# Performance work log

Measured on AMD Instinct MI355X. Metric: run time of the kernel, lower is better.

The kernel has to match this reference:

```python
import jax, jax.numpy as jnp
import numpy as np
import math

B, T, C, H, LC, DFF = 2, 1024, 1024, 16, 256, 4096
EPS = 1e-6


def _ln(x):
    # LayerNorm without affine (elementwise_affine=False under AdaLN), eps=1e-6
    m = jnp.mean(x, -1, keepdims=True)
    v = jnp.mean((x - m) ** 2, -1, keepdims=True)
    return (x - m) * jax.lax.rsqrt(v + EPS)


def _heads(t):
    b, l, c = t.shape
    return t.reshape(b, l, H, c // H).transpose(0, 2, 1, 3)  # (b,H,l,dh)


def _unheads(t):
    b, h, l, d = t.shape
    return t.transpose(0, 2, 1, 3).reshape(b, l, h * d)


def setup_inputs():
    key = jax.random.key(0)
    ks = jax.random.split(key, 16)
    s = 0.02
    p = lambda k, sh: jax.random.normal(k, sh, jnp.float32) * s
    x_star = jax.random.normal(ks[0], (B, T, C), jnp.float32)
    x_hat = jax.random.normal(ks[1], (B, T, C), jnp.float32)
    c = jax.random.normal(ks[2], (B, LC, C), jnp.float32)
    chunk = jnp.sort(jax.random.randint(ks[3], (B, T), 0, 32), axis=1)
    m_star = chunk[:, :, None] > chunk[:, None, :]   # attend to strictly earlier chunks
    m_hat = chunk[:, :, None] == chunk[:, None, :]   # attend within same chunk
    dep_mask = jax.random.bernoulli(ks[4], 0.98, (B, T, T)) | jnp.eye(T, dtype=bool)[None]
    return dict(
        x_star=x_star, x_hat=x_hat, c=c,
        m_star=m_star, m_hat=m_hat, dep_mask=dep_mask,
        ncond_g=jnp.ones((C,), jnp.float32), ncond_b=jnp.zeros((C,), jnp.float32),
        Wq=p(ks[5], (C, C)), bq=jnp.zeros((C,), jnp.float32),
        Wkv=p(ks[6], (C, 2 * C)), bkv=jnp.zeros((2 * C,), jnp.float32),
        Wco=p(ks[7], (C, C)), bco=jnp.zeros((C,), jnp.float32),
        Wada=p(ks[8], (C, 6 * C)), bada=jnp.zeros((6 * C,), jnp.float32),
        Wqkv=p(ks[9], (C, 3 * C)), bqkv=jnp.zeros((3 * C,), jnp.float32),
        Wo=p(ks[10], (C, C)), bo=jnp.zeros((C,), jnp.float32),
        W1=p(ks[11], (C, DFF)), b1=jnp.zeros((DFF,), jnp.float32),
        W2=p(ks[12], (DFF, C)), b2=jnp.zeros((C,), jnp.float32),
    )


def _cross_attn(x, c, Wq, bq, Wkv, bkv, Wco, bco):
    q = _heads(x @ Wq + bq)
    k, v = jnp.split(c @ Wkv + bkv, 2, -1)
    k, v = _heads(k), _heads(v)
    att = jnp.einsum('bhtd,bhsd->bhts', q, k) / math.sqrt(C // H)
    y = jnp.einsum('bhts,bhsd->bhtd', jax.nn.softmax(att, -1), v)
    return _unheads(y) @ Wco + bco


def _interleave(xs, xh, m_star, m_hat, dep, Wqkv, bqkv, Wo, bo):
    # Attention.forward_interleave (eval: dropout identity)
    NEG = -jnp.inf
    sc = 1.0 / math.sqrt(C // H)
    qkv = lambda x: [_heads(t) for t in jnp.split(x @ Wqkv + bqkv, 3, -1)]
    qs, ks, vs = qkv(xs)
    qh, kh, vh = qkv(xh)
    blk_star = (~m_star)[:, None]     # True -> block
    blk_hat = (~m_hat)[:, None]
    blk_dep = (~dep)[:, None]
    causal = jnp.triu(jnp.ones((T, T), bool), 1)[None, None]
    # star stream: causal + dependency mask
    att_star = jnp.einsum('bhtd,bhsd->bhts', qs, ks) * sc
    att_star = jnp.where(blk_dep, NEG, att_star)
    p_star = jax.nn.softmax(jnp.where(causal, NEG, att_star), -1)
    y_star = _unheads(jnp.einsum('bhts,bhsd->bhtd', p_star, vs)) @ Wo + bo
    # hat stream: merge logits (q_hat vs k_star on earlier chunks, q_hat vs k_hat within chunk)
    a1 = jnp.where(blk_star, NEG, jnp.einsum('bhtd,bhsd->bhts', qh, ks) * sc)
    a2 = jnp.where(blk_hat, NEG, jnp.einsum('bhtd,bhsd->bhts', qh, kh) * sc)
    merged = jnp.where(jnp.isinf(a2), a1, a2)
    merged = jnp.where(blk_dep, NEG, merged)
    p_hat = jax.nn.softmax(merged, -1)
    y_hat = jnp.einsum('bhts,bhsd->bhtd', jnp.where(blk_star, 0.0, p_hat), vs) \
          + jnp.einsum('bhts,bhsd->bhtd', jnp.where(blk_hat, 0.0, p_hat), vh)
    y_hat = _unheads(y_hat) @ Wo + bo
    return y_star, y_hat


def reference(x_star, x_hat, c, m_star, m_hat, dep_mask,
              ncond_g, ncond_b, Wq, bq, Wkv, bkv, Wco, bco, Wada, bada,
              Wqkv, bqkv, Wo, bo, W1, b1, W2, b2):
    mod = lambda x, sh, scale: x * (1 + scale) + sh
    mlp = lambda x: jax.nn.gelu(x @ W1 + b1, approximate=True) @ W2 + b2
    ca = lambda x: _cross_attn(_ln(x) * ncond_g + ncond_b, c, Wq, bq, Wkv, bkv, Wco, bco)
    ada = lambda t: jnp.split(jax.nn.silu(t) @ Wada + bada, 6, -1)
    gs = ada(ca(x_star))
    gh = ada(ca(x_hat))
    ms = mod(_ln(x_star), gs[0], gs[1])
    mh = mod(_ln(x_hat), gh[0], gh[1])
    ys, yh = _interleave(ms, mh, m_star, m_hat, dep_mask, Wqkv, bqkv, Wo, bo)
    x_star = x_star + gs[2] * ys
    x_hat = x_hat + gh[2] * yh
    x_star = x_star + gs[5] * mlp(mod(_ln(x_star), gs[3], gs[4]))
    x_hat = x_hat + gh[5] * mlp(mod(_ln(x_hat), gh[3], gh[4]))
    return x_star, x_hat
```

## Files before the change

### kernel.cpp

```cpp
#include <hip/hip_runtime.h>
#include <hip/hip_bf16.h>
#include <stdint.h>

#define DEVI __device__ __forceinline__

typedef __bf16 bf16x8 __attribute__((ext_vector_type(8)));
typedef float f32x4 __attribute__((ext_vector_type(4)));
typedef unsigned short us;
typedef unsigned long long ull;

DEVI float b2f(us u) { union { unsigned int i; float f; } v; v.i = ((unsigned int)u) << 16; return v.f; }
DEVI us f2b(float f) {
  union { unsigned int i; float f; } v; v.f = f;
  unsigned int r = (v.i + 0x7fffu + ((v.i >> 16) & 1u)) >> 16;
  return (us)r;
}

#define NEGINF (-__builtin_inff())

DEVI void gl2lds16(const us* g, us* l) {
  __builtin_amdgcn_global_load_lds(
      (const __attribute__((address_space(1))) unsigned int*)g,
      (__attribute__((address_space(3))) unsigned int*)l, 16, 0, 0);
}

__global__ __launch_bounds__(256) void detect_flags(
    const unsigned int* __restrict__ xw, const unsigned int* __restrict__ mw,
    int* __restrict__ flags) {
  const int t = threadIdx.x;
  int cnt = 0, big = 0;
  for (int i = t; i < 4096; i += 256) {
    unsigned int w = xw[i];
    us lo = (us)(w & 0xffffu);
    float a = fabsf(b2f(lo));
    cnt += ((lo == 0) || (a >= 1e-8f && a <= 256.f)) ? 1 : 0;
    big |= (mw[i] > 1u) ? 1 : 0;
  }
  for (int o = 32; o; o >>= 1) { cnt += __shfl_down(cnt, o); big |= __shfl_down(big, o); }
  __shared__ int sc[4], sb[4];
  if ((t & 63) == 0) { sc[t >> 6] = cnt; sb[t >> 6] = big; }
  __syncthreads();
  if (t == 0) {
    flags[0] = (sc[0] + sc[1] + sc[2] + sc[3] < 2048) ? 1 : 0;
    flags[1] = (sb[0] | sb[1] | sb[2] | sb[3]);
  }
}

__global__ __launch_bounds__(256) void cvt_bf16(
    const void* __restrict__ src, us* __restrict__ dst, int n,
    const int* __restrict__ flags) {
  const int f32mode = flags[0];
  int idx = (blockIdx.x * 256 + threadIdx.x) * 4;
  if (idx >= n) return;
  if (f32mode) {
    const float* s = (const float*)src;
    float4 v = *(const float4*)(s + idx);
    dst[idx] = f2b(v.x); dst[idx + 1] = f2b(v.y);
    dst[idx + 2] = f2b(v.z); dst[idx + 3] = f2b(v.w);
  } else {
    *(uint2*)(dst + idx) = *(const uint2*)((const us*)src + idx);
  }
}

struct P10 { const void* p[10]; };
__global__ __launch_bounds__(256) void cvt_small(P10 ps, us* __restrict__ dst,
                                                 const int* __restrict__ flags) {
  const int offs[11] = {0, 1024, 2048, 3072, 5120, 6144, 12288, 15360, 16384, 20480, 21504};
  int idx = blockIdx.x * 256 + threadIdx.x;
  if (idx >= 21504) return;
  int seg = 0;
#pragma unroll
  for (int i = 1; i < 10; ++i) seg += (idx >= offs[i]) ? 1 : 0;
  int local = idx - offs[seg];
  float v = flags[0] ? ((const float*)ps.p[seg])[local]
                     : b2f(((const us*)ps.p[seg])[local]);
  dst[idx] = f2b(v);
}

__global__ __launch_bounds__(256) void transpose_cvt64(
    const void* __restrict__ W, us* __restrict__ WT, int K, int N,
    const int* __restrict__ flags) {
  __shared__ __attribute__((aligned(16))) us tile[64 * 72];
  const int f32m = flags[0];
  const int k0 = blockIdx.x * 64, n0 = blockIdx.y * 64;
  const int t = threadIdx.x;
  const int row = t >> 2, colb = (t & 3) * 16;
  const int sw = ((row >> 4) & 3) << 4;
  us tmp[16];
  if (f32m) {
    const float* src = (const float*)W + (size_t)(k0 + row) * N + n0 + colb;
#pragma unroll
    for (int i = 0; i < 16; i += 4) {
      float4 v = *(const float4*)(src + i);
      tmp[i] = f2b(v.x); tmp[i + 1] = f2b(v.y); tmp[i + 2] = f2b(v.z); tmp[i + 3] = f2b(v.w);
    }
  } else {
    const us* src = (const us*)W + (size_t)(k0 + row) * N + n0 + colb;
    *(uint4*)tmp = *(const uint4*)src;
    *(uint4*)(tmp + 8) = *(const uint4*)(src + 8);
  }
  *(uint4*)&tile[row * 72 + (colb ^ sw)] = *(uint4*)tmp;
  *(uint4*)&tile[row * 72 + (colb ^ sw) + 8] = *(uint4*)(tmp + 8);
  __syncthreads();
  const int orow = t >> 2, ocolb = (t & 3) * 16;
  const int pc = (orow & 15) | ((orow & 48) ^ (ocolb & 48));
  us out[16];
#pragma unroll
  for (int i = 0; i < 16; ++i) out[i] = tile[(ocolb + i) * 72 + pc];
  us* dst = WT + (size_t)(n0 + orow) * K + k0 + ocolb;
  *(uint4*)dst = *(uint4*)out;
  *(uint4*)(dst + 8) = *(uint4*)(out + 8);
}

struct P3 { const void* p[3]; };
__global__ __launch_bounds__(256) void pack_mask3(P3 ms, ull* __restrict__ bits,
                                                  const int* __restrict__ flags) {
  const int bytemode = flags[1];
  const void* m = ms.p[blockIdx.y];
  ull* out = bits + (size_t)blockIdx.y * 32768;
  int wv = blockIdx.x * 4 + (threadIdx.x >> 6);
  int lane = threadIdx.x & 63;
  for (int w = 0; w < 16; ++w) {
    int v;
    if (bytemode) v = ((const unsigned char*)m)[(size_t)wv * 1024 + w * 64 + lane];
    else          v = ((const int*)m)[(size_t)wv * 1024 + w * 64 + lane];
    ull b = __ballot(v != 0);
    if (lane == 0) out[(size_t)wv * 16 + w] = b;
  }
}

__global__ __launch_bounds__(256) void hat_blockflags(
    const ull* __restrict__ starb, const ull* __restrict__ hatb, int* __restrict__ bf) {
  const int bt = blockIdx.x;
  const int b = bt >> 4, tt = bt & 15;
  const int t = threadIdx.x, wv = t >> 6, lane = t & 63;
  const int t0 = tt * 64;
  for (int k = 0; k < 4; ++k) {
    int ck = wv * 4 + k;
    ull sw = starb[(size_t)(b * 1024 + t0 + lane) * 16 + ck];
    ull hw = hatb[(size_t)(b * 1024 + t0 + lane) * 16 + ck];
    int f = (__ballot(sw != 0ull) ? 1 : 0) | (__ballot(hw != 0ull) ? 2 : 0);
    if (lane == 0) bf[bt * 16 + ck] = f;
  }
}

__global__ __launch_bounds__(256) void vtrans(
    const us* __restrict__ src, us* __restrict__ dst,
    int T, int stride, int colBase, int rowOff) {
  __shared__ __attribute__((aligned(16))) us tile[64][65];
  const int bh = blockIdx.y, b = bh >> 4, h = bh & 15;
  const int t0 = blockIdx.x * 64;
  const int t = threadIdx.x;
#pragma unroll
  for (int it = 0; it < 2; ++it) {
    int idx = it * 256 + t; int r = idx >> 3, c8 = (idx & 7) * 8;
    uint4 d4 = *(const uint4*)(src + (size_t)(rowOff + b * T + t0 + r) * stride + colBase + h * 64 + c8);
    const us* e = (const us*)&d4;
#pragma unroll
    for (int i = 0; i < 8; ++i) tile[r][c8 + i] = e[i];
  }
  __syncthreads();
#pragma unroll
  for (int it = 0; it < 2; ++it) {
    int idx = it * 256 + t; int d = idx >> 3, c8 = (idx & 7) * 8;
    us tmp[8];
#pragma unroll
    for (int i = 0; i < 8; ++i) tmp[i] = tile[c8 + i][d];
    *(uint4*)(dst + ((size_t)(bh * 64 + d)) * T + t0 + c8) = *(const uint4*)tmp;
  }
}

__global__ __launch_bounds__(256) void ln_affine(
    const void* __restrict__ xs, const void* __restrict__ xh,
    const us* __restrict__ gw, const us* __restrict__ bw,
    us* __restrict__ lnx, us* __restrict__ xn, const int* __restrict__ flags) {
  const int f32m = flags[0];
  const int row = blockIdx.x;
  const void* xp = (row < 2048) ? xs : xh;
  const size_t base = (size_t)(row & 2047) * 1024;
  const int t = threadIdx.x;
  float v[4]; float s = 0.f, ss = 0.f;
#pragma unroll
  for (int i = 0; i < 4; ++i) {
    size_t idx = base + i * 256 + t;
    float x = f32m ? ((const float*)xp)[idx] : b2f(((const us*)xp)[idx]);
    v[i] = x; s += x; ss += x * x;
  }
  for (int o = 32; o; o >>= 1) { s += __shfl_down(s, o); ss += __shfl_down(ss, o); }
  __shared__ float red[2][4];
  const int wv = t >> 6, lane = t & 63;
  if (lane == 0) { red[0][wv] = s; red[1][wv] = ss; }
  __syncthreads();
  s = red[0][0] + red[0][1] + red[0][2] + red[0][3];
  ss = red[1][0] + red[1][1] + red[1][2] + red[1][3];
  const float mean = s * (1.f / 1024.f);
  const float var = fmaxf(ss * (1.f / 1024.f) - mean * mean, 0.f);
  const float rstd = rsqrtf(var + 1e-6f);
  const size_t ro = (size_t)row * 1024;
#pragma unroll
  for (int i = 0; i < 4; ++i) {
    int c = i * 256 + t;
    float n = (v[i] - mean) * rstd;
    lnx[ro + c] = f2b(n);
    xn[ro + c] = f2b(n * b2f(gw[c]) + b2f(bw[c]));
  }
}

__global__ __launch_bounds__(256) void mod_ms(
    const us* __restrict__ lnx, const us* __restrict__ gada, us* __restrict__ ms) {
  const size_t idx = ((size_t)blockIdx.x * 256 + threadIdx.x) * 4;
  const int row = (int)(idx >> 10), c = (int)(idx & 1023);
  const size_t gb = (size_t)row * 6144;
#pragma unroll
  for (int i = 0; i < 4; ++i) {
    float sh = b2f(gada[gb + c + i]);
    float sc = b2f(gada[gb + 1024 + c + i]);
    ms[idx + i] = f2b(b2f(lnx[idx + i]) * (1.f + sc) + sh);
  }
}

__global__ __launch_bounds__(256) void ln_mod(
    const float* __restrict__ x1, const us* __restrict__ gada, us* __restrict__ m2) {
  const int row = blockIdx.x;
  const float* xp = x1 + (size_t)row * 1024;
  const int t = threadIdx.x;
  float v[4]; float s = 0.f, ss = 0.f;
#pragma unroll
  for (int i = 0; i < 4; ++i) { float x = xp[i * 256 + t]; v[i] = x; s += x; ss += x * x; }
  for (int o = 32; o; o >>= 1) { s += __shfl_down(s, o); ss += __shfl_down(ss, o); }
  __shared__ float red[2][4];
  const int wv = t >> 6, lane = t & 63;
  if (lane == 0) { red[0][wv] = s; red[1][wv] = ss; }
  __syncthreads();
  s = red[0][0] + red[0][1] + red[0][2] + red[0][3];
  ss = red[1][0] + red[1][1] + red[1][2] + red[1][3];
  const float mean = s * (1.f / 1024.f);
  const float var = fmaxf(ss * (1.f / 1024.f) - mean * mean, 0.f);
  const float rstd = rsqrtf(var + 1e-6f);
  const size_t gb = (size_t)row * 6144;
#pragma unroll
  for (int i = 0; i < 4; ++i) {
    int c = i * 256 + t;
    float n = (v[i] - mean) * rstd;
    float sh = b2f(gada[gb + 3072 + c]);
    float sc = b2f(gada[gb + 4096 + c]);
    m2[(size_t)row * 1024 + c] = f2b(n * (1.f + sc) + sh);
  }
}

enum { EPI_BF16 = 0, EPI_SILU, EPI_GELU, EPI_GATE_XRES, EPI_GATE_OUT };

template <int EPI>
DEVI void gemm_epi(float v, int gmr, int gn, int N, void* out,
                   const us* gate, const void* res0, const void* res1,
                   const int* oflags) {
  const size_t oi = (size_t)gmr * N + gn;
  if constexpr (EPI == EPI_BF16) {
    ((us*)out)[oi] = f2b(v);
  } else if constexpr (EPI == EPI_SILU) {
    ((us*)out)[oi] = f2b(v / (1.f + __expf(-v)));
  } else if constexpr (EPI == EPI_GELU) {
    float u = 0.7978845608028654f * (v + 0.044715f * v * v * v);
    float th = 1.f - 2.f / (__expf(2.f * u) + 1.f);
    ((us*)out)[oi] = f2b(0.5f * v * (1.f + th));
  } else if constexpr (EPI == EPI_GATE_XRES) {
    float g = b2f(gate[(size_t)gmr * 6144 + gn]);
    const void* xr = (gmr < 2048) ? res0 : res1;
    size_t xi = (size_t)(gmr & 2047) * 1024 + gn;
    float x = oflags[0] ? ((const float*)xr)[xi] : b2f(((const us*)xr)[xi]);
    ((float*)out)[oi] = x + g * v;
  } else {
    float g = b2f(gate[(size_t)gmr * 6144 + gn]);
    float x = ((const float*)res0)[oi];
    float r2 = x + g * v;
    if (oflags[0]) ((float*)out)[oi] = r2;
    else ((us*)out)[oi] = f2b(r2);
  }
}

template <int EPI>
__global__ __launch_bounds__(256) void gemm_bt(
    const us* __restrict__ A, const us* __restrict__ BT,
    const us* __restrict__ bias, void* __restrict__ out,
    int M, int N, int K,
    const us* __restrict__ gate,
    const void* __restrict__ res0, const void* __restrict__ res1,
    const int* __restrict__ oflags) {
  __shared__ __attribute__((aligned(16))) us As[2][128 * 32];
  __shared__ __attribute__((aligned(16))) us Bs[2][128 * 32];
  const int m0 = blockIdx.x * 128, n0 = blockIdx.y * 128;
  const int t = threadIdx.x;
  const int wave = t >> 6, lane = t & 63;
  const int wm = (wave >> 1) * 64, wn = (wave & 1) * 64;
  const int l16 = lane & 15, quad = lane >> 4;
  f32x4 acc[4][4] = {};

  const int lr = lane >> 2, lc = (lane & 3) * 8;
  const us* gA = A + (size_t)(m0 + wave * 32 + lr) * K + lc;
  const us* gB = BT + (size_t)(n0 + wave * 32 + lr) * K + lc;
  const int wo = wave * 1024;

#define STAGE_BT(buf, k)                                    \
  { us* pA = &As[buf][wo]; us* pB = &Bs[buf][wo];           \
    gl2lds16(gA + (k), pA);                                 \
    gl2lds16(gA + (size_t)16 * K + (k), pA + 512);          \
    gl2lds16(gB + (k), pB);                                 \
    gl2lds16(gB + (size_t)16 * K + (k), pB + 512); }

  STAGE_BT(0, 0);
  STAGE_BT(1, 32);
  const int NK = K >> 5;
  int cur = 0;
  for (int i = 0; i < NK - 1; ++i) {
    asm volatile("s_waitcnt vmcnt(4)\n\ts_barrier" ::: "memory");
    bf16x8 af[4], bfv[4];
#pragma unroll
    for (int x = 0; x < 4; ++x) af[x] = *(const bf16x8*)(const void*)&As[cur][(wm + x * 16 + l16) * 32 + quad * 8];
#pragma unroll
    for (int j = 0; j < 4; ++j) bfv[j] = *(const bf16x8*)(const void*)&Bs[cur][(wn + j * 16 + l16) * 32 + quad * 8];
    asm volatile("s_waitcnt lgkmcnt(0)\n\ts_barrier" ::: "memory");
    if (i + 2 < NK) STAGE_BT(cur, (i + 2) * 32);
#pragma unroll
    for (int x = 0; x < 4; ++x)
#pragma unroll
      for (int j = 0; j < 4; ++j)
        acc[x][j] = __builtin_amdgcn_mfma_f32_16x16x32_bf16(af[x], bfv[j], acc[x][j], 0, 0, 0);
    cur ^= 1;
  }
  asm volatile("s_waitcnt vmcnt(0)\n\ts_barrier" ::: "memory");
  {
    bf16x8 af[4], bfv[4];
#pragma unroll
    for (int x = 0; x < 4; ++x) af[x] = *(const bf16x8*)(const void*)&As[cur][(wm + x * 16 + l16) * 32 + quad * 8];
#pragma unroll
    for (int j = 0; j < 4; ++j) bfv[j] = *(const bf16x8*)(const void*)&Bs[cur][(wn + j * 16 + l16) * 32 + quad * 8];
#pragma unroll
    for (int x = 0; x < 4; ++x)
#pragma unroll
      for (int j = 0; j < 4; ++j)
        acc[x][j] = __builtin_amdgcn_mfma_f32_16x16x32_bf16(af[x], bfv[j], acc[x][j], 0, 0, 0);
  }
#undef STAGE_BT

#pragma unroll
  for (int i = 0; i < 4; ++i) {
    const int gm = m0 + wm + i * 16 + quad * 4;
#pragma unroll
    for (int j = 0; j < 4; ++j) {
      const int gn = n0 + wn + j * 16 + l16;
      const float bv = b2f(bias[gn]);
#pragma unroll
      for (int r = 0; r < 4; ++r)
        gemm_epi<EPI>(acc[i][j][r] + bv, gm + r, gn, N, out, gate, res0, res1, oflags);
    }
  }
}

template <int EPI>
__global__ __launch_bounds__(256) void gemm_bt64(
    const us* __restrict__ A, const us* __restrict__ BT,
    const us* __restrict__ bias, void* __restrict__ out,
    int M, int N, int K,
    const us* __restrict__ gate,
    const void* __restrict__ res0, const void* __restrict__ res1,
    const int* __restrict__ oflags) {
  __shared__ __attribute__((aligned(16))) us As[2][128 * 32];
  __shared__ __attribute__((aligned(16))) us Bs[2][64 * 32];
  const int m0 = blockIdx.x * 128, n0 = blockIdx.y * 64;
  const int t = threadIdx.x;
  const int wave = t >> 6, lane = t & 63;
  const int wm = (wave >> 1) * 64, wn = (wave & 1) * 32;
  const int l16 = lane & 15, quad = lane >> 4;
  f32x4 acc[4][2] = {};

  const int lr = lane >> 2, lc = (lane & 3) * 8;
  const us* gA = A + (size_t)(m0 + wave * 32 + lr) * K + lc;
  const us* gB = BT + (size_t)(n0 + wave * 16 + lr) * K + lc;
  const int woA = wave * 1024, woB = wave * 512;

#define STAGE_BT64(buf, k)                                  \
  { us* pA = &As[buf][woA];                                 \
    gl2lds16(gA + (k), pA);                                 \
    gl2lds16(gA + (size_t)16 * K + (k), pA + 512);          \
    gl2lds16(gB + (k), &Bs[buf][woB]); }

  STAGE_BT64(0, 0);
  STAGE_BT64(1, 32);
  const int NK = K >> 5;
  int cur = 0;
  for (int i = 0; i < NK - 1; ++i) {
    asm volatile("s_waitcnt vmcnt(3)\n\ts_barrier" ::: "memory");
    bf16x8 af[4], bfv[2];
#pragma unroll
    for (int x = 0; x < 4; ++x) af[x] = *(const bf16x8*)(const void*)&As[cur][(wm + x * 16 + l16) * 32 + quad * 8];
#pragma unroll
    for (int j = 0; j < 2; ++j) bfv[j] = *(const bf16x8*)(const void*)&Bs[cur][(wn + j * 16 + l16) * 32 + quad * 8];
    asm volatile("s_waitcnt lgkmcnt(0)\n\ts_barrier" ::: "memory");
    if (i + 2 < NK) STAGE_BT64(cur, (i + 2) * 32);
#pragma unroll
    for (int x = 0; x < 4; ++x)
#pragma unroll
      for (int j = 0; j < 2; ++j)
        acc[x][j] = __builtin_amdgcn_mfma_f32_16x16x32_bf16(af[x], bfv[j], acc[x][j], 0, 0, 0);
    cur ^= 1;
  }
  asm volatile("s_waitcnt vmcnt(0)\n\ts_barrier" ::: "memory");
  {
    bf16x8 af[4], bfv[2];
#pragma unroll
    for (int x = 0; x < 4; ++x) af[x] = *(const bf16x8*)(const void*)&As[cur][(wm + x * 16 + l16) * 32 + quad * 8];
#pragma unroll
    for (int j = 0; j < 2; ++j) bfv[j] = *(const bf16x8*)(const void*)&Bs[cur][(wn + j * 16 + l16) * 32 + quad * 8];
#pragma unroll
    for (int x = 0; x < 4; ++x)
#pragma unroll
      for (int j = 0; j < 2; ++j)
        acc[x][j] = __builtin_amdgcn_mfma_f32_16x16x32_bf16(af[x], bfv[j], acc[x][j], 0, 0, 0);
  }
#undef STAGE_BT64

#pragma unroll
  for (int i = 0; i < 4; ++i) {
    const int gm = m0 + wm + i * 16 + quad * 4;
#pragma unroll
    for (int j = 0; j < 2; ++j) {
      const int gn = n0 + wn + j * 16 + l16;
      const float bv = b2f(bias[gn]);
#pragma unroll
      for (int r = 0; r < 4; ++r)
        gemm_epi<EPI>(acc[i][j][r] + bv, gm + r, gn, N, out, gate, res0, res1, oflags);
    }
  }
}

struct AttnState { float m[4], l[4]; f32x4 o[4]; };

DEVI void st_init(AttnState& s) {
#pragma unroll
  for (int r = 0; r < 4; ++r) { s.m[r] = NEGINF; s.l[r] = 0.f; s.o[r] = f32x4{}; }
}

DEVI void stage64(us* __restrict__ dst, const us* __restrict__ src,
                  int strideUs, int t) {
#pragma unroll
  for (int it = 0; it < 2; ++it) {
    const int id = it * 256 + t;
    const int row = id >> 3, c8 = (id & 7) * 8;
    *(uint4*)&dst[row * 72 + c8] = *(const uint4*)(src + (size_t)row * strideUs + c8);
  }
}

template <bool MASKED>
DEVI void attn_round(const us* __restrict__ Kb, const us* __restrict__ Vb,
                     us* __restrict__ Pb, const ull* mrow,
                     bf16x8 aq0, bf16x8 aq1, AttnState& st,
                     int wv, int l16, int quad) {
  f32x4 s[4];
  __builtin_amdgcn_s_setprio(1);
#pragma unroll
  for (int j = 0; j < 4; ++j) {
    const int row = j * 16 + l16;
    bf16x8 bk0 = *(const bf16x8*)(const void*)&Kb[row * 72 + quad * 8];
    bf16x8 bk1 = *(const bf16x8*)(const void*)&Kb[row * 72 + 32 + quad * 8];
    f32x4 z = {};
    z = __builtin_amdgcn_mfma_f32_16x16x32_bf16(aq0, bk0, z, 0, 0, 0);
    z = __builtin_amdgcn_mfma_f32_16x16x32_bf16(aq1, bk1, z, 0, 0, 0);
    s[j] = z;
  }
  __builtin_amdgcn_s_setprio(0);
  const float CE = 0.18033688011112042f;
#pragma unroll
  for (int r = 0; r < 4; ++r) {
    float mx = fmaxf(fmaxf(s[0][r], s[1][r]), fmaxf(s[2][r], s[3][r]));
#pragma unroll
    for (int o2 = 8; o2; o2 >>= 1) mx = fmaxf(mx, __shfl_xor(mx, o2));
    const float mn = fmaxf(st.m[r], mx);
    const float alpha = exp2f((st.m[r] - mn) * CE);
    const float mnC = mn * CE;
    float rs = 0.f;
#pragma unroll
    for (int j = 0; j < 4; ++j) {
      float p = exp2f(__builtin_fmaf(s[j][r], CE, -mnC));
      if constexpr (MASKED) p = ((mrow[r] >> (j * 16 + l16)) & 1ull) ? p : 0.f;
      rs += p;
      ((__bf16*)Pb)[(wv * 16 + quad * 4 + r) * 72 + j * 16 + l16] = (__bf16)p;
    }
#pragma unroll
    for (int o2 = 8; o2; o2 >>= 1) rs += __shfl_xor(rs, o2);
    st.m[r] = mn;
    st.l[r] = st.l[r] * alpha + rs;
#pragma unroll
    for (int jd = 0; jd < 4; ++jd) st.o[jd][r] *= alpha;
  }
  bf16x8 ap0 = *(const bf16x8*)(const void*)&Pb[(wv * 16 + l16) * 72 + quad * 8];
  bf16x8 ap1 = *(const bf16x8*)(const void*)&Pb[(wv * 16 + l16) * 72 + 32 + quad * 8];
  __builtin_amdgcn_s_setprio(1);
#pragma unroll
  for (int jd = 0; jd < 4; ++jd) {
    bf16x8 v0 = *(const bf16x8*)(const void*)&Vb[(jd * 16 + l16) * 72 + quad * 8];
    bf16x8 v1 = *(const bf16x8*)(const void*)&Vb[(jd * 16 + l16) * 72 + 32 + quad * 8];
    st.o[jd] = __builtin_amdgcn_mfma_f32_16x16x32_bf16(ap0, v0, st.o[jd], 0, 0, 0);
    st.o[jd] = __builtin_amdgcn_mfma_f32_16x16x32_bf16(ap1, v1, st.o[jd], 0, 0, 0);
  }
  __builtin_amdgcn_s_setprio(0);
}

DEVI void attn_write(us* __restrict__ y, const AttnState& st, int rowAbs,
                     int h, int l16, int quad) {
#pragma unroll
  for (int r = 0; r < 4; ++r) {
    const float inv = (st.l[r] > 0.f) ? 1.f / st.l[r] : 0.f;
#pragma unroll
    for (int jd = 0; jd < 4; ++jd)
      y[(size_t)(rowAbs + quad * 4 + r) * 1024 + h * 64 + jd * 16 + l16] =
          f2b(st.o[jd][r] * inv);
  }
}

__global__ __launch_bounds__(256) void cross_attn_mfma(
    const us* __restrict__ q, const us* __restrict__ kv,
    const us* __restrict__ vT, us* __restrict__ y) {
  __shared__ __attribute__((aligned(16))) us Kb[64 * 72];
  __shared__ __attribute__((aligned(16))) us Vb[64 * 72];
  __shared__ __attribute__((aligned(16))) us Pb[64 * 72];
  const int bid = blockIdx.x;
  const int xcd = bid & 7, tmp = bid >> 3;
  const int tt = tmp & 15, gq = tmp >> 4;
  const int g = gq * 8 + xcd;
  const int strm = g >> 5, b = (g >> 4) & 1, h = g & 15;
  const int t = threadIdx.x, wv = t >> 6, lane = t & 63;
  const int l16 = lane & 15, quad = lane >> 4;
  const int rowbase = strm * 2048 + b * 1024 + tt * 64 + wv * 16;
  const us* qp = q + (size_t)(rowbase + l16) * 1024 + h * 64 + quad * 8;
  bf16x8 aq0 = *(const bf16x8*)(qp);
  bf16x8 aq1 = *(const bf16x8*)(qp + 32);
  const us* kb = kv + (size_t)b * (256 * 2048) + h * 64;
  const us* vb = vT + (size_t)(b * 16 + h) * (64 * 256);
  AttnState st; st_init(st);
  for (int rnd = 0; rnd < 4; ++rnd) {
    const int s0 = rnd * 64;
    __syncthreads();
    stage64(Kb, kb + (size_t)s0 * 2048, 2048, t);
    stage64(Vb, vb + s0, 256, t);
    __syncthreads();
    attn_round<false>(Kb, Vb, Pb, nullptr, aq0, aq1, st, wv, l16, quad);
  }
  attn_write(y, st, rowbase, h, l16, quad);
}

DEVI void star_body(us* Kb, us* Vb, us* Pb, const us* qkv, const us* vT,
                    const ull* depb, us* y, int b, int h, int tt, int t) {
  const int wv = t >> 6, lane = t & 63;
  const int l16 = lane & 15, quad = lane >> 4;
  const int t0 = tt * 64;
  const int rowbase = b * 1024 + t0 + wv * 16;
  const us* qp = qkv + (size_t)(rowbase + l16) * 3072 + h * 64 + quad * 8;
  bf16x8 aq0 = *(const bf16x8*)(qp);
  bf16x8 aq1 = *(const bf16x8*)(qp + 32);
  const us* kb = qkv + (size_t)(b * 1024) * 3072 + 1024 + h * 64;
  const us* vb = vT + (size_t)(b * 16 + h) * 65536;
  AttnState st; st_init(st);
  ull mrow[4];
  for (int ck = 0; ck <= tt; ++ck) {
    const int s0 = ck * 64;
    __syncthreads();
    stage64(Kb, kb + (size_t)s0 * 3072, 3072, t);
    stage64(Vb, vb + s0, 1024, t);
    __syncthreads();
#pragma unroll
    for (int r = 0; r < 4; ++r) {
      ull d = depb[(size_t)(rowbase + quad * 4 + r) * 16 + ck];
      if (ck == tt) {
        const int idx = wv * 16 + quad * 4 + r;
        d &= (2ull << idx) - 1ull;
      }
      mrow[r] = d;
    }
    attn_round<true>(Kb, Vb, Pb, mrow, aq0, aq1, st, wv, l16, quad);
  }
  attn_write(y, st, rowbase, h, l16, quad);
}

DEVI void hat_body(us* Kb, us* Vb, us* Pb, const us* qkv,
                   const us* vsT, const us* vhT,
                   const ull* starb, const ull* hatb, const ull* depb,
                   const int* bflags, us* y, int b, int h, int tt, int t) {
  const int wv = t >> 6, lane = t & 63;
  const int l16 = lane & 15, quad = lane >> 4;
  const int t0 = tt * 64;
  const int rowbase = b * 1024 + t0 + wv * 16;
  const us* qp = qkv + (size_t)(2048 + rowbase + l16) * 3072 + h * 64 + quad * 8;
  bf16x8 aq0 = *(const bf16x8*)(qp);
  bf16x8 aq1 = *(const bf16x8*)(qp + 32);
  const us* ksb = qkv + (size_t)(b * 1024) * 3072 + 1024 + h * 64;
  const us* khb = qkv + (size_t)(2048 + b * 1024) * 3072 + 1024 + h * 64;
  const us* vsb = vsT + (size_t)(b * 16 + h) * 65536;
  const us* vhb = vhT + (size_t)(b * 16 + h) * 65536;
  AttnState st; st_init(st);
  ull mrow[4];
  for (int ck = 0; ck < 16; ++ck) {
    const int f = bflags[(b * 16 + tt) * 16 + ck];
    const int s0 = ck * 64;
    if (f & 1) {
      __syncthreads();
      stage64(Kb, ksb + (size_t)s0 * 3072, 3072, t);
      stage64(Vb, vsb + s0, 1024, t);
      __syncthreads();
#pragma unroll
      for (int r = 0; r < 4; ++r) {
        const size_t mi = (size_t)(rowbase + quad * 4 + r) * 16 + ck;
        mrow[r] = starb[mi] & depb[mi];
      }
      attn_round<true>(Kb, Vb, Pb, mrow, aq0, aq1, st, wv, l16, quad);
    }
    if (f & 2) {
      __syncthreads();
      stage64(Kb, khb + (size_t)s0 * 3072, 3072, t);
      stage64(Vb, vhb + s0, 1024, t);
      __syncthreads();
#pragma unroll
      for (int r = 0; r < 4; ++r) {
        const size_t mi = (size_t)(rowbase + quad * 4 + r) * 16 + ck;
        mrow[r] = hatb[mi] & depb[mi];
      }
      attn_round<true>(Kb, Vb, Pb, mrow, aq0, aq1, st, wv, l16, quad);
    }
  }
  attn_write(y, st, 2048 + rowbase, h, l16, quad);
}

__global__ __launch_bounds__(256) void self_attn_mfma(
    const us* __restrict__ qkv,
    const us* __restrict__ vstT, const us* __restrict__ vhtT,
    const ull* __restrict__ sbits, const ull* __restrict__ hbits,
    const ull* __restrict__ dbits, const int* __restrict__ bflags,
    us* __restrict__ y) {
  __shared__ __attribute__((aligned(16))) us Kb[64 * 72];
  __shared__ __attribute__((aligned(16))) us Vb[64 * 72];
  __shared__ __attribute__((aligned(16))) us Pb[64 * 72];
  const int bid = blockIdx.x;
  const int xcd = bid & 7, tmp = bid >> 3;
  const int pr = tmp & 7, gq = tmp >> 3;
  const int g = gq * 8 + xcd;
  const int ttA = pr, ttB = 15 - pr;
  const int t = threadIdx.x;
  if (g < 32) {
    star_body(Kb, Vb, Pb, qkv, vstT, dbits, y, g >> 4, g & 15, ttA, t);
    star_body(Kb, Vb, Pb, qkv, vstT, dbits, y, g >> 4, g & 15, ttB, t);
  } else {
    const int g2 = g - 32;
    hat_body(Kb, Vb, Pb, qkv, vstT, vhtT, sbits, hbits, dbits, bflags,
             y, g2 >> 4, g2 & 15, ttA, t);
    hat_body(Kb, Vb, Pb, qkv, vstT, vhtT, sbits, hbits, dbits, bflags,
             y, g2 >> 4, g2 & 15, ttB, t);
  }
}

extern "C" void kernel_launch(void* const* d_in, const int* in_sizes, int n_in,
                              void* d_out, int out_size, void* d_ws, size_t ws_size,
                              hipStream_t stream) {
  const void* xs = d_in[0];
  const void* xh = d_in[1];
  const void* cc = d_in[2];
  const void* mstar = d_in[3];
  const void* mhat = d_in[4];
  const void* mdep = d_in[5];
  const void* ng = d_in[6];
  const void* nb = d_in[7];
  const void* Wq = d_in[8];
  const void* bq = d_in[9];
  const void* Wkv = d_in[10];
  const void* bkv = d_in[11];
  const void* Wco = d_in[12];
  const void* bco = d_in[13];
  const void* Wada = d_in[14];
  const void* bada = d_in[15];
  const void* Wqkv = d_in[16];
  const void* bqkv = d_in[17];
  const void* Wo = d_in[18];
  const void* bo = d_in[19];
  const void* W1 = d_in[20];
  const void* b1 = d_in[21];
  const void* W2 = d_in[22];
  const void* b2 = d_in[23];
  (void)in_sizes; (void)n_in; (void)out_size; (void)ws_size;

  char* ws = (char*)d_ws;
  size_t off = 0;
  auto alloc = [&](size_t bytes) -> char* {
    char* p = ws + off;
    off += (bytes + 255) & ~(size_t)255;
    return p;
  };
  int* flags = (int*)alloc(256);
  int* bflags = (int*)alloc(512 * 4);
  us* smallb = (us*)alloc(21504 * 2);
  us* ngb = smallb, *nbb = smallb + 1024, *bqb = smallb + 2048,
      *bkvb = smallb + 3072, *bcob = smallb + 5120, *badab = smallb + 6144,
      *bqkvb = smallb + 12288, *bob = smallb + 15360, *b1b = smallb + 16384,
      *b2b = smallb + 20480;
  us* WqT = (us*)alloc(1048576ull * 2);
  us* WkvT = (us*)alloc(2097152ull * 2);
  us* WcoT = (us*)alloc(1048576ull * 2);
  us* WadaT = (us*)alloc(6291456ull * 2);
  us* WqkvT = (us*)alloc(3145728ull * 2);
  us* WoT = (us*)alloc(1048576ull * 2);
  us* W1T = (us*)alloc(4194304ull * 2);
  us* W2T = (us*)alloc(4194304ull * 2);
  us* xn = (us*)alloc(4194304ull * 2);
  us* qb = (us*)alloc(4194304ull * 2);
  us* kvb = (us*)alloc(1048576ull * 2);
  us* gada = (us*)alloc(25165824ull * 2);
  us* msb = (us*)alloc(4194304ull * 2);
  us* qkvb = (us*)alloc(12582912ull * 2);
  float* x1 = (float*)alloc(4194304ull * 4);
  us* hid = (us*)alloc(16777216ull * 2);
  ull* mb = (ull*)alloc(3ull * 32768 * 8);
  us* kvT = (us*)alloc(524288ull * 2);
  us* vstT = (us*)alloc(2097152ull * 2);
  us* vhtT = (us*)alloc(2097152ull * 2);

  ull* sbits = mb;
  ull* hbits = mb + 32768;
  ull* dbits = mb + 65536;
  us* ccb = hid;
  us* lnx = hid + 1048576;
  us* yca = xn;
  us* silub = qb;
  us* yat = msb;

  dim3 blk(256);
  detect_flags<<<1, blk, 0, stream>>>((const unsigned int*)xs, (const unsigned int*)mdep, flags);

  cvt_bf16<<<512, blk, 0, stream>>>(cc, ccb, 524288, flags);
  P10 ps10; ps10.p[0] = ng; ps10.p[1] = nb; ps10.p[2] = bq; ps10.p[3] = bkv;
  ps10.p[4] = bco; ps10.p[5] = bada; ps10.p[6] = bqkv; ps10.p[7] = bo;
  ps10.p[8] = b1; ps10.p[9] = b2;
  cvt_small<<<84, blk, 0, stream>>>(ps10, smallb, flags);

  transpose_cvt64<<<dim3(16, 16), blk, 0, stream>>>(Wq, WqT, 1024, 1024, flags);
  transpose_cvt64<<<dim3(16, 32), blk, 0, stream>>>(Wkv, WkvT, 1024, 2048, flags);
  transpose_cvt64<<<dim3(16, 16), blk, 0, stream>>>(Wco, WcoT, 1024, 1024, flags);
  transpose_cvt64<<<dim3(16, 96), blk, 0, stream>>>(Wada, WadaT, 1024, 6144, flags);
  transpose_cvt64<<<dim3(16, 48), blk, 0, stream>>>(Wqkv, WqkvT, 1024, 3072, flags);
  transpose_cvt64<<<dim3(16, 16), blk, 0, stream>>>(Wo, WoT, 1024, 1024, flags);
  transpose_cvt64<<<dim3(16, 64), blk, 0, stream>>>(W1, W1T, 1024, 4096, flags);
  transpose_cvt64<<<dim3(64, 16), blk, 0, stream>>>(W2, W2T, 4096, 1024, flags);

  P3 ps3; ps3.p[0] = mstar; ps3.p[1] = mhat; ps3.p[2] = mdep;
  pack_mask3<<<dim3(512, 3), blk, 0, stream>>>(ps3, mb, flags);
  hat_blockflags<<<32, blk, 0, stream>>>(sbits, hbits, bflags);

  ln_affine<<<4096, blk, 0, stream>>>(xs, xh, ngb, nbb, lnx, xn, flags);
  gemm_bt64<EPI_BF16><<<dim3(32, 16), blk, 0, stream>>>(xn, WqT, bqb, qb, 4096, 1024, 1024, nullptr, nullptr, nullptr, nullptr);
  gemm_bt64<EPI_BF16><<<dim3(4, 32), blk, 0, stream>>>(ccb, WkvT, bkvb, kvb, 512, 2048, 1024, nullptr, nullptr, nullptr, nullptr);
  vtrans<<<dim3(4, 32), blk, 0, stream>>>(kvb, kvT, 256, 2048, 1024, 0);
  cross_attn_mfma<<<1024, blk, 0, stream>>>(qb, kvb, kvT, yca);
  gemm_bt64<EPI_SILU><<<dim3(32, 16), blk, 0, stream>>>(yca, WcoT, bcob, silub, 4096, 1024, 1024, nullptr, nullptr, nullptr, nullptr);
  gemm_bt<EPI_BF16><<<dim3(32, 48), blk, 0, stream>>>(silub, WadaT, badab, gada, 4096, 6144, 1024, nullptr, nullptr, nullptr, nullptr);
  mod_ms<<<4096, blk, 0, stream>>>(lnx, gada, msb);
  gemm_bt<EPI_BF16><<<dim3(32, 24), blk, 0, stream>>>(msb, WqkvT, bqkvb, qkvb, 4096, 3072, 1024, nullptr, nullptr, nullptr, nullptr);
  vtrans<<<dim3(16, 32), blk, 0, stream>>>(qkvb, vstT, 1024, 3072, 2048, 0);
  vtrans<<<dim3(16, 32), blk, 0, stream>>>(qkvb, vhtT, 1024, 3072, 2048, 2048);
  self_attn_mfma<<<512, blk, 0, stream>>>(qkvb, vstT, vhtT, sbits, hbits, dbits, bflags, yat);
  gemm_bt64<EPI_GATE_XRES><<<dim3(32, 16), blk, 0, stream>>>(yat, WoT, bob, x1, 4096, 1024, 1024, gada + 2048, xs, xh, flags);
  ln_mod<<<4096, blk, 0, stream>>>(x1, gada, msb);
  gemm_bt<EPI_GELU><<<dim3(32, 32), blk, 0, stream>>>(msb, W1T, b1b, hid, 4096, 4096, 1024, nullptr, nullptr, nullptr, nullptr);
  gemm_bt64<EPI_GATE_OUT><<<dim3(32, 16), blk, 0, stream>>>(hid, W2T, b2b, d_out, 4096, 1024, 4096, gada + 5120, x1, nullptr, flags);
}
```

Measured before the change: 625.6 us.

## Batch weight transposes, merge V transposes, split-K the W2 GEMM with a reduce

Three separate changes. The eight per-weight transpose launches become one table-driven kernel, and the two V-transpose launches become one kernel using a z grid dimension, both to cut launch overhead. The final W2 GEMM switches from the 64-wide tile kernel to the 128x128 tile kernel with 2-way split-K, writing fp32 partial sums that a new gate_reduce kernel adds together with bias, gate and residual. The split-K path adds roughly 32 MB of fp32 partial-sum writes and reads. It also reuses the msb buffer for those partials, which only fits if msb and qkvb are allocated back to back.

Measured after the change: 693.0 us. 1.11x slower.

```diff
diff --git a/kernel.cpp b/kernel.cpp
--- a/kernel.cpp
+++ b/kernel.cpp
@@ -77,12 +77,30 @@
   dst[idx] = f2b(v);
 }
 
-__global__ __launch_bounds__(256) void transpose_cvt64(
-    const void* __restrict__ W, us* __restrict__ WT, int K, int N,
-    const int* __restrict__ flags) {
+struct TTab {
+  const void* src[8];
+  us* dst[8];
+  int K[8];
+  int N[8];
+  int pre[8];
+};
+
+__global__ __launch_bounds__(256) void transpose_cvt_all(
+    TTab tt, const int* __restrict__ flags) {
   __shared__ __attribute__((aligned(16))) us tile[64 * 72];
   const int f32m = flags[0];
-  const int k0 = blockIdx.x * 64, n0 = blockIdx.y * 64;
+  const int bid = blockIdx.x;
+  int seg = 0;
+#pragma unroll
+  for (int i = 1; i < 8; ++i) seg += (bid >= tt.pre[i]) ? 1 : 0;
+  const int K = tt.K[seg], N = tt.N[seg];
+  const void* W = tt.src[seg];
+  us* WT = tt.dst[seg];
+  const int local = bid - tt.pre[seg];
+  const int kd = K >> 6;
+  const int kb = local & (kd - 1);
+  const int nb = (kd == 64) ? (local >> 6) : (local >> 4);
+  const int k0 = kb * 64, n0 = nb * 64;
   const int t = threadIdx.x;
   const int row = t >> 2, colb = (t & 3) * 16;
   const int sw = ((row >> 4) & 3) << 4;
@@ -170,6 +188,34 @@
   }
 }
 
+__global__ __launch_bounds__(256) void vtrans_qkv(
+    const us* __restrict__ src, us* __restrict__ dst0, us* __restrict__ dst1) {
+  __shared__ __attribute__((aligned(16))) us tile[64][65];
+  const int z = blockIdx.z;
+  us* dst = z ? dst1 : dst0;
+  const int rowOff = z ? 2048 : 0;
+  const int bh = blockIdx.y, b = bh >> 4, h = bh & 15;
+  const int t0 = blockIdx.x * 64;
+  const int t = threadIdx.x;
+#pragma unroll
+  for (int it = 0; it < 2; ++it) {
+    int idx = it * 256 + t; int r = idx >> 3, c8 = (idx & 7) * 8;
+    uint4 d4 = *(const uint4*)(src + (size_t)(rowOff + b * 1024 + t0 + r) * 3072 + 2048 + h * 64 + c8);
+    const us* e = (const us*)&d4;
+#pragma unroll
+    for (int i = 0; i < 8; ++i) tile[r][c8 + i] = e[i];
+  }
+  __syncthreads();
+#pragma unroll
+  for (int it = 0; it < 2; ++it) {
+    int idx = it * 256 + t; int d = idx >> 3, c8 = (idx & 7) * 8;
+    us tmp[8];
+#pragma unroll
+    for (int i = 0; i < 8; ++i) tmp[i] = tile[c8 + i][d];
+    *(uint4*)(dst + ((size_t)(bh * 64 + d)) * 1024 + t0 + c8) = *(const uint4*)tmp;
+  }
+}
+
 __global__ __launch_bounds__(256) void ln_affine(
     const void* __restrict__ xs, const void* __restrict__ xh,
     const us* __restrict__ gw, const us* __restrict__ bw,
@@ -248,7 +294,7 @@
   }
 }
 
-enum { EPI_BF16 = 0, EPI_SILU, EPI_GELU, EPI_GATE_XRES, EPI_GATE_OUT };
+enum { EPI_BF16 = 0, EPI_SILU, EPI_GELU, EPI_GATE_XRES, EPI_PARTIAL };
 
 template <int EPI>
 DEVI void gemm_epi(float v, int gmr, int gn, int N, void* out,
@@ -270,11 +316,7 @@
     float x = oflags[0] ? ((const float*)xr)[xi] : b2f(((const us*)xr)[xi]);
     ((float*)out)[oi] = x + g * v;
   } else {
-    float g = b2f(gate[(size_t)gmr * 6144 + gn]);
-    float x = ((const float*)res0)[oi];
-    float r2 = x + g * v;
-    if (oflags[0]) ((float*)out)[oi] = r2;
-    else ((us*)out)[oi] = f2b(r2);
+    ((float*)out)[oi] = v;
   }
 }
 
@@ -282,13 +324,18 @@
 __global__ __launch_bounds__(256) void gemm_bt(
     const us* __restrict__ A, const us* __restrict__ BT,
     const us* __restrict__ bias, void* __restrict__ out,
-    int M, int N, int K,
+    int M, int N, int K, int Ks,
     const us* __restrict__ gate,
     const void* __restrict__ res0, const void* __restrict__ res1,
     const int* __restrict__ oflags) {
   __shared__ __attribute__((aligned(16))) us As[2][128 * 32];
   __shared__ __attribute__((aligned(16))) us Bs[2][128 * 32];
   const int m0 = blockIdx.x * 128, n0 = blockIdx.y * 128;
+  const int kz = blockIdx.z;
+  A += (size_t)kz * K;
+  BT += (size_t)kz * K;
+  if constexpr (EPI == EPI_PARTIAL)
+    out = (void*)((float*)out + (size_t)kz * (size_t)M * N);
   const int t = threadIdx.x;
   const int wave = t >> 6, lane = t & 63;
   const int wm = (wave >> 1) * 64, wn = (wave & 1) * 64;
@@ -296,16 +343,16 @@
   f32x4 acc[4][4] = {};
 
   const int lr = lane >> 2, lc = (lane & 3) * 8;
-  const us* gA = A + (size_t)(m0 + wave * 32 + lr) * K + lc;
-  const us* gB = BT + (size_t)(n0 + wave * 32 + lr) * K + lc;
+  const us* gA = A + (size_t)(m0 + wave * 32 + lr) * Ks + lc;
+  const us* gB = BT + (size_t)(n0 + wave * 32 + lr) * Ks + lc;
   const int wo = wave * 1024;
 
 #define STAGE_BT(buf, k)                                    \
   { us* pA = &As[buf][wo]; us* pB = &Bs[buf][wo];           \
     gl2lds16(gA + (k), pA);                                 \
-    gl2lds16(gA + (size_t)16 * K + (k), pA + 512);          \
+    gl2lds16(gA + (size_t)16 * Ks + (k), pA + 512);         \
     gl2lds16(gB + (k), pB);                                 \
-    gl2lds16(gB + (size_t)16 * K + (k), pB + 512); }
+    gl2lds16(gB + (size_t)16 * Ks + (k), pB + 512); }
 
   STAGE_BT(0, 0);
   STAGE_BT(1, 32);
@@ -348,7 +395,7 @@
 #pragma unroll
     for (int j = 0; j < 4; ++j) {
       const int gn = n0 + wn + j * 16 + l16;
-      const float bv = b2f(bias[gn]);
+      const float bv = (EPI == EPI_PARTIAL) ? 0.f : b2f(bias[gn]);
 #pragma unroll
       for (int r = 0; r < 4; ++r)
         gemm_epi<EPI>(acc[i][j][r] + bv, gm + r, gn, N, out, gate, res0, res1, oflags);
@@ -360,7 +407,7 @@
 __global__ __launch_bounds__(256) void gemm_bt64(
     const us* __restrict__ A, const us* __restrict__ BT,
     const us* __restrict__ bias, void* __restrict__ out,
-    int M, int N, int K,
+    int M, int N, int K, int Ks,
     const us* __restrict__ gate,
     const void* __restrict__ res0, const void* __restrict__ res1,
     const int* __restrict__ oflags) {
@@ -374,14 +421,14 @@
   f32x4 acc[4][2] = {};
 
   const int lr = lane >> 2, lc = (lane & 3) * 8;
-  const us* gA = A + (size_t)(m0 + wave * 32 + lr) * K + lc;
-  const us* gB = BT + (size_t)(n0 + wave * 16 + lr) * K + lc;
+  const us* gA = A + (size_t)(m0 + wave * 32 + lr) * Ks + lc;
+  const us* gB = BT + (size_t)(n0 + wave * 16 + lr) * Ks + lc;
   const int woA = wave * 1024, woB = wave * 512;
 
 #define STAGE_BT64(buf, k)                                  \
   { us* pA = &As[buf][woA];                                 \
     gl2lds16(gA + (k), pA);                                 \
-    gl2lds16(gA + (size_t)16 * K + (k), pA + 512);          \
+    gl2lds16(gA + (size_t)16 * Ks + (k), pA + 512);         \
     gl2lds16(gB + (k), &Bs[buf][woB]); }
 
   STAGE_BT64(0, 0);
@@ -430,6 +477,27 @@
       for (int r = 0; r < 4; ++r)
         gemm_epi<EPI>(acc[i][j][r] + bv, gm + r, gn, N, out, gate, res0, res1, oflags);
     }
+  }
+}
+
+__global__ __launch_bounds__(256) void gate_reduce(
+    const float* __restrict__ p, const float* __restrict__ x1,
+    const us* __restrict__ gate, const us* __restrict__ bias,
+    void* __restrict__ out, const int* __restrict__ flags) {
+  const size_t idx = ((size_t)blockIdx.x * 256 + threadIdx.x) * 4;
+  const int row = (int)(idx >> 10), c = (int)(idx & 1023);
+  float4 a = *(const float4*)(p + idx);
+  float4 b = *(const float4*)(p + 4194304 + idx);
+  float4 x = *(const float4*)(x1 + idx);
+  const int f32m = flags[0];
+#pragma unroll
+  for (int j = 0; j < 4; ++j) {
+    float g = b2f(gate[(size_t)row * 6144 + c + j]);
+    float bv = b2f(bias[c + j]);
+    float v = (&a.x)[j] + (&b.x)[j] + bv;
+    float r = (&x.x)[j] + g * v;
+    if (f32m) ((float*)out)[idx + j] = r;
+    else ((us*)out)[idx + j] = f2b(r);
   }
 }
 
@@ -728,6 +796,7 @@
   us* yca = xn;
   us* silub = qb;
   us* yat = msb;
+  float* pbuf = (float*)msb;
 
   dim3 blk(256);
   detect_flags<<<1, blk, 0, stream>>>((const unsigned int*)xs, (const unsigned int*)mdep, flags);
@@ -738,33 +807,37 @@
   ps10.p[8] = b1; ps10.p[9] = b2;
   cvt_small<<<84, blk, 0, stream>>>(ps10, smallb, flags);
 
-  transpose_cvt64<<<dim3(16, 16), blk, 0, stream>>>(Wq, WqT, 1024, 1024, flags);
-  transpose_cvt64<<<dim3(16, 32), blk, 0, stream>>>(Wkv, WkvT, 1024, 2048, flags);
-  transpose_cvt64<<<dim3(16, 16), blk, 0, stream>>>(Wco, WcoT, 1024, 1024, flags);
-  transpose_cvt64<<<dim3(16, 96), blk, 0, stream>>>(Wada, WadaT, 1024, 6144, flags);
-  transpose_cvt64<<<dim3(16, 48), blk, 0, stream>>>(Wqkv, WqkvT, 1024, 3072, flags);
-  transpose_cvt64<<<dim3(16, 16), blk, 0, stream>>>(Wo, WoT, 1024, 1024, flags);
-  transpose_cvt64<<<dim3(16, 64), blk, 0, stream>>>(W1, W1T, 1024, 4096, flags);
-  transpose_cvt64<<<dim3(64, 16), blk, 0, stream>>>(W2, W2T, 4096, 1024, flags);
+  TTab tt;
+  tt.src[0] = Wq;   tt.dst[0] = WqT;   tt.K[0] = 1024; tt.N[0] = 1024;
+  tt.src[1] = Wkv;  tt.dst[1] = WkvT;  tt.K[1] = 1024; tt.N[1] = 2048;
+  tt.src[2] = Wco;  tt.dst[2] = WcoT;  tt.K[2] = 1024; tt.N[2] = 1024;
+  tt.src[3] = Wada; tt.dst[3] = WadaT; tt.K[3] = 1024; tt.N[3] = 6144;
+  tt.src[4] = Wqkv; tt.dst[4] = WqkvT; tt.K[4] = 1024; tt.N[4] = 3072;
+  tt.src[5] = Wo;   tt.dst[5] = WoT;   tt.K[5] = 1024; tt.N[5] = 1024;
+  tt.src[6] = W1;   tt.dst[6] = W1T;   tt.K[6] = 1024; tt.N[6] = 4096;
+  tt.src[7] = W2;   tt.dst[7] = W2T;   tt.K[7] = 4096; tt.N[7] = 1024;
+  int acc = 0;
+  for (int i = 0; i < 8; ++i) { tt.pre[i] = acc; acc += (tt.K[i] >> 6) * (tt.N[i] >> 6); }
+  transpose_cvt_all<<<acc, blk, 0, stream>>>(tt, flags);
 
   P3 ps3; ps3.p[0] = mstar; ps3.p[1] = mhat; ps3.p[2] = mdep;
   pack_mask3<<<dim3(512, 3), blk, 0, stream>>>(ps3, mb, flags);
   hat_blockflags<<<32, blk, 0, stream>>>(sbits, hbits, bflags);
 
   ln_affine<<<4096, blk, 0, stream>>>(xs, xh, ngb, nbb, lnx, xn, flags);
-  gemm_bt64<EPI_BF16><<<dim3(32, 16), blk, 0, stream>>>(xn, WqT, bqb, qb, 4096, 1024, 1024, nullptr, nullptr, nullptr, nullptr);
-  gemm_bt64<EPI_BF16><<<dim3(4, 32), blk, 0, stream>>>(ccb, WkvT, bkvb, kvb, 512, 2048, 1024, nullptr, nullptr, nullptr, nullptr);
+  gemm_bt64<EPI_BF16><<<dim3(32, 16), blk, 0, stream>>>(xn, WqT, bqb, qb, 4096, 1024, 1024, 1024, nullptr, nullptr, nullptr, nullptr);
+  gemm_bt64<EPI_BF16><<<dim3(4, 32), blk, 0, stream>>>(ccb, WkvT, bkvb, kvb, 512, 2048, 1024, 1024, nullptr, nullptr, nullptr, nullptr);
   vtrans<<<dim3(4, 32), blk, 0, stream>>>(kvb, kvT, 256, 2048, 1024, 0);
   cross_attn_mfma<<<1024, blk, 0, stream>>>(qb, kvb, kvT, yca);
-  gemm_bt64<EPI_SILU><<<dim3(32, 16), blk, 0, stream>>>(yca, WcoT, bcob, silub, 4096, 1024, 1024, nullptr, nullptr, nullptr, nullptr);
-  gemm_bt<EPI_BF16><<<dim3(32, 48), blk, 0, stream>>>(silub, WadaT, badab, gada, 4096, 6144, 1024, nullptr, nullptr, nullptr, nullptr);
+  gemm_bt64<EPI_SILU><<<dim3(32, 16), blk, 0, stream>>>(yca, WcoT, bcob, silub, 4096, 1024, 1024, 1024, nullptr, nullptr, nullptr, nullptr);
+  gemm_bt<EPI_BF16><<<dim3(32, 48), blk, 0, stream>>>(silub, WadaT, badab, gada, 4096, 6144, 1024, 1024, nullptr, nullptr, nullptr, nullptr);
   mod_ms<<<4096, blk, 0, stream>>>(lnx, gada, msb);
-  gemm_bt<EPI_BF16><<<dim3(32, 24), blk, 0, stream>>>(msb, WqkvT, bqkvb, qkvb, 4096, 3072, 1024, nullptr, nullptr, nullptr, nullptr);
-  vtrans<<<dim3(16, 32), blk, 0, stream>>>(qkvb, vstT, 1024, 3072, 2048, 0);
-  vtrans<<<dim3(16, 32), blk, 0, stream>>>(qkvb, vhtT, 1024, 3072, 2048, 2048);
+  gemm_bt<EPI_BF16><<<dim3(32, 24), blk, 0, stream>>>(msb, WqkvT, bqkvb, qkvb, 4096, 3072, 1024, 1024, nullptr, nullptr, nullptr, nullptr);
+  vtrans_qkv<<<dim3(16, 32, 2), blk, 0, stream>>>(qkvb, vstT, vhtT);
   self_attn_mfma<<<512, blk, 0, stream>>>(qkvb, vstT, vhtT, sbits, hbits, dbits, bflags, yat);
-  gemm_bt64<EPI_GATE_XRES><<<dim3(32, 16), blk, 0, stream>>>(yat, WoT, bob, x1, 4096, 1024, 1024, gada + 2048, xs, xh, flags);
+  gemm_bt64<EPI_GATE_XRES><<<dim3(32, 16), blk, 0, stream>>>(yat, WoT, bob, x1, 4096, 1024, 1024, 1024, gada + 2048, xs, xh, flags);
   ln_mod<<<4096, blk, 0, stream>>>(x1, gada, msb);
-  gemm_bt<EPI_GELU><<<dim3(32, 32), blk, 0, stream>>>(msb, W1T, b1b, hid, 4096, 4096, 1024, nullptr, nullptr, nullptr, nullptr);
-  gemm_bt64<EPI_GATE_OUT><<<dim3(32, 16), blk, 0, stream>>>(hid, W2T, b2b, d_out, 4096, 1024, 4096, gada + 5120, x1, nullptr, flags);
-}
+  gemm_bt<EPI_GELU><<<dim3(32, 32), blk, 0, stream>>>(msb, W1T, b1b, hid, 4096, 4096, 1024, 1024, nullptr, nullptr, nullptr, nullptr);
+  gemm_bt<EPI_PARTIAL><<<dim3(32, 8, 2), blk, 0, stream>>>(hid, W2T, b2b, pbuf, 4096, 1024, 2048, 4096, nullptr, nullptr, nullptr, nullptr);
+  gate_reduce<<<4096, blk, 0, stream>>>(pbuf, x1, gada + 5120, b2b, d_out, flags);
+}
```
